# Kernel tuning notes

Measured on AMD Instinct MI355X. Metric: run time of the kernel, lower is better.

## Reference

```python
import jax, jax.numpy as jnp
import numpy as np

N, E, B = 50000, 600000, 512
IN, HID, META = 128, 128, 27


def _gcn_layer(h_in, W, b, src, dst, norm, n_nodes):
    # GCNConv: out = scatter_add_{dst}( norm * (x W)[src] ) + b
    h = h_in @ W  # [N, HID]
    msg = h[src] * norm[:, None]  # [E+N, HID] gather + scale
    out = jax.ops.segment_sum(msg, dst, num_segments=n_nodes)
    return out + b


def setup_inputs() -> dict:
    key = jax.random.key(0)
    ks = jax.random.split(key, 16)
    x = jax.random.normal(ks[0], (N, IN), dtype=jnp.float32)
    edge_index = jax.random.randint(ks[1], (2, E), 0, N, dtype=jnp.int64)
    batch = jnp.sort(jax.random.randint(ks[2], (N,), 0, B, dtype=jnp.int64))
    metadata = jax.random.normal(ks[3], (B, META), dtype=jnp.float32)
    def glorot(k, shape):
        lim = np.sqrt(6.0 / (shape[0] + shape[1]))
        return jax.random.uniform(k, shape, jnp.float32, -lim, lim)
    params = {
        'W1': glorot(ks[4], (IN, HID)),  'b1': jnp.zeros((HID,), jnp.float32),
        'W2': glorot(ks[5], (HID, HID)), 'b2': jnp.zeros((HID,), jnp.float32),
        'W3': glorot(ks[6], (HID, HID)), 'b3': jnp.zeros((HID,), jnp.float32),
        'Wh1': glorot(ks[7], (HID + META, HID)), 'bh1': jnp.zeros((HID,), jnp.float32),
        'Wh2': glorot(ks[8], (HID, 1)),  'bh2': jnp.zeros((1,), jnp.float32),
    }
    return {'x': x, 'edge_index': edge_index, 'batch': batch, 'metadata': metadata, **params}


def reference(x, edge_index, batch, metadata, W1, b1, W2, b2, W3, b3, Wh1, bh1, Wh2, bh2):
    n_nodes = x.shape[0]
    # add self loops (PyG GCNConv default)
    loops = jnp.arange(n_nodes, dtype=edge_index.dtype)
    src = jnp.concatenate([edge_index[0], loops])
    dst = jnp.concatenate([edge_index[1], loops])
    # symmetric degree normalization D^{-1/2} A_hat D^{-1/2}
    deg = jax.ops.segment_sum(jnp.ones_like(dst, dtype=x.dtype), dst, num_segments=n_nodes)
    dinv = jax.lax.rsqrt(jnp.maximum(deg, 1.0))  # self-loops guarantee deg >= 1
    norm = dinv[src] * dinv[dst]  # [E+N]
    h = jax.nn.relu(_gcn_layer(x, W1, b1, src, dst, norm, n_nodes))
    h = jax.nn.relu(_gcn_layer(h, W2, b2, src, dst, norm, n_nodes))
    h = jax.nn.relu(_gcn_layer(h, W3, b3, src, dst, norm, n_nodes))
    # global mean pool over graphs
    n_graphs = metadata.shape[0]
    summed = jax.ops.segment_sum(h, batch, num_segments=n_graphs)  # [B, HID]
    counts = jax.ops.segment_sum(jnp.ones((n_nodes,), x.dtype), batch, num_segments=n_graphs)
    emb = summed / jnp.maximum(counts, 1.0)[:, None]
    # MLP head
    z = jnp.concatenate([emb, metadata], axis=1)  # [B, HID+META]
    z = jax.nn.relu(z @ Wh1 + bh1)
    return z @ Wh2 + bh2  # [B, 1] raw logits
```

## Files before the change

kernel.cpp:

```cpp
#include <hip/hip_runtime.h>

#define NN 50000
#define NE 600000
#define NB 512
#define HD 128
#define NMETA 27
#define SCAN_BLOCKS ((NN + 255) / 256)

typedef __attribute__((ext_vector_type(8))) short short8;
typedef __attribute__((ext_vector_type(4))) float f32x4;

__device__ __forceinline__ float relu(float x) { return fmaxf(x, 0.0f); }

__device__ __forceinline__ unsigned short f2bf(float f) {
    unsigned u = __float_as_uint(f);
    unsigned r = u + 0x7FFFu + ((u >> 16) & 1u);
    return (unsigned short)(r >> 16);
}
__device__ __forceinline__ float bf2f(unsigned short v) {
    return __uint_as_float(((unsigned)v) << 16);
}

__global__ __launch_bounds__(256) void k_count(const int* __restrict__ dst, int* __restrict__ cnt) {
    int i = blockIdx.x * 256 + threadIdx.x;
    if (i < NE) atomicAdd(&cnt[dst[i]], 1);
}

__global__ __launch_bounds__(256) void k_scanA(const int* __restrict__ cnt, int* __restrict__ partial,
                                               int* __restrict__ blocksum, float* __restrict__ dinv) {
    const int t = threadIdx.x;
    const int i = blockIdx.x * 256 + t;
    int v = (i < NN) ? cnt[i] : 0;
    if (i < NN) dinv[i] = rsqrtf((float)v + 1.0f);
    __shared__ int s[256];
    s[t] = v;
    __syncthreads();
    for (int off = 1; off < 256; off <<= 1) {
        int u = (t >= off) ? s[t - off] : 0;
        __syncthreads();
        s[t] += u;
        __syncthreads();
    }
    if (i < NN) partial[i] = s[t] - v;
    if (t == 255) blocksum[blockIdx.x] = s[255];
}

__global__ __launch_bounds__(256) void k_scanB(const int* __restrict__ blocksum, int* __restrict__ blockoff) {
    const int t = threadIdx.x;
    int v = (t < SCAN_BLOCKS) ? blocksum[t] : 0;
    __shared__ int s[256];
    s[t] = v;
    __syncthreads();
    for (int off = 1; off < 256; off <<= 1) {
        int u = (t >= off) ? s[t - off] : 0;
        __syncthreads();
        s[t] += u;
        __syncthreads();
    }
    if (t < SCAN_BLOCKS) blockoff[t] = s[t] - v;
}

__global__ __launch_bounds__(256) void k_scanC(const int* __restrict__ partial, const int* __restrict__ blockoff,
                                               int* __restrict__ rowptr, int* __restrict__ cursor) {
    const int i = blockIdx.x * 256 + threadIdx.x;
    if (i < NN) {
        int rp = partial[i] + blockoff[i >> 8];
        rowptr[i] = rp;
        cursor[i] = rp;
    }
    if (i == 0) rowptr[NN] = NE;
}

__global__ __launch_bounds__(256) void k_fill(const int* __restrict__ src, const int* __restrict__ dst,
                                              int* __restrict__ cursor, int* __restrict__ csr_src) {
    int e = blockIdx.x * 256 + threadIdx.x;
    if (e >= NE) return;
    int s = src[e], d = dst[e];
    int pos = atomicAdd(&cursor[d], 1);
    csr_src[pos] = s;
}

__global__ __launch_bounds__(256) void k_castWt3(const float* __restrict__ W1, const float* __restrict__ W2,
                                                 const float* __restrict__ W3, unsigned short* __restrict__ Wt1,
                                                 unsigned short* __restrict__ Wt2, unsigned short* __restrict__ Wt3) {
    int i = blockIdx.x * 256 + threadIdx.x;
    if (i >= 3 * HD * HD) return;
    int which = i / (HD * HD);
    int r = i - which * (HD * HD);
    int k = r >> 7, n = r & 127;
    const float* W = (which == 0) ? W1 : (which == 1) ? W2 : W3;
    unsigned short* Wt = (which == 0) ? Wt1 : (which == 1) ? Wt2 : Wt3;
    Wt[n * HD + k] = f2bf(W[r]);
}

__global__ __launch_bounds__(256) void k_gemm_x(const float* __restrict__ X,
                                                const unsigned short* __restrict__ Wt,
                                                const float* __restrict__ dinv,
                                                unsigned short* __restrict__ T) {
    __shared__ unsigned short Ws[HD * HD];
    char* wsb = (char*)Ws;
    for (int i = threadIdx.x; i < HD * HD / 8; i += 256) {
        short8 v = ((const short8*)Wt)[i];
        int byte = i * 16;
        *(short8*)(wsb + (byte ^ (((byte >> 8) & 7) << 4))) = v;
    }
    __syncthreads();

    const int wave = threadIdx.x >> 6;
    const int lane = threadIdx.x & 63;
    const int lr = lane & 15;
    const int kh = lane >> 4;
    const int r0 = blockIdx.x * 64 + wave * 16;
    const float* arow = X + (size_t)min(r0 + lr, NN - 1) * HD + kh * 8;

    f32x4 acc[8] = {};
#pragma unroll
    for (int kk = 0; kk < 4; ++kk) {
        float4 a0 = *reinterpret_cast<const float4*>(arow + kk * 32);
        float4 a1 = *reinterpret_cast<const float4*>(arow + kk * 32 + 4);
        short8 af;
        af[0] = (short)f2bf(a0.x); af[1] = (short)f2bf(a0.y);
        af[2] = (short)f2bf(a0.z); af[3] = (short)f2bf(a0.w);
        af[4] = (short)f2bf(a1.x); af[5] = (short)f2bf(a1.y);
        af[6] = (short)f2bf(a1.z); af[7] = (short)f2bf(a1.w);
#pragma unroll
        for (int n = 0; n < 8; ++n) {
            int byte = (n * 16 + lr) * 256 + kk * 64 + kh * 16;
            short8 bf = *(const short8*)(wsb + (byte ^ (((byte >> 8) & 7) << 4)));
            acc[n] = __builtin_amdgcn_mfma_f32_16x16x32_bf16(af, bf, acc[n], 0, 0, 0);
        }
    }
    float dv[4];
#pragma unroll
    for (int r = 0; r < 4; ++r) {
        int row = r0 + kh * 4 + r;
        dv[r] = (row < NN) ? dinv[row] : 0.0f;
    }
#pragma unroll
    for (int n = 0; n < 8; ++n) {
#pragma unroll
        for (int r = 0; r < 4; ++r) {
            int row = r0 + kh * 4 + r;
            if (row < NN) T[(size_t)row * HD + n * 16 + lr] = f2bf(acc[n][r] * dv[r]);
        }
    }
}

template <int MODE>
__global__ __launch_bounds__(512, 8) void k_fused(const int* __restrict__ rowptr, const int* __restrict__ csr_src,
                                                  const unsigned short* __restrict__ Tin, const float* __restrict__ dinv,
                                                  const float* __restrict__ b, const unsigned short* __restrict__ Wt,
                                                  unsigned short* __restrict__ Out, const int* __restrict__ batch,
                                                  float* __restrict__ embsum) {
    __shared__ char smem[32 * 132 * 4 + 128];
    char* hsb = smem;
    float* hsf = (float*)smem;
    int* sg = (int*)(smem + 32 * 132 * 4);

    const int rl  = threadIdx.x >> 4;
    const int l16 = threadIdx.x & 15;
    const int row = blockIdx.x * 32 + rl;
    const int c   = l16 * 8;

    if (MODE == 2 && threadIdx.x < 32) {
        int rr = blockIdx.x * 32 + threadIdx.x;
        sg[threadIdx.x] = (rr < NN) ? batch[rr] : -1;
    }

    float acc[8] = {};

    if (row < NN) {
        const int lo = rowptr[row], hi = rowptr[row + 1];
        int j = lo;
        int sA0, sA1, sA2, sA3, sB0, sB1, sB2, sB3;
        bool haveA = (j + 3 < hi);
        if (haveA) { sA0 = csr_src[j]; sA1 = csr_src[j + 1]; sA2 = csr_src[j + 2]; sA3 = csr_src[j + 3]; }
        while (haveA) {
            const int jn = j + 4;
            const bool haveB = (jn + 3 < hi);
            if (haveB) { sB0 = csr_src[jn]; sB1 = csr_src[jn + 1]; sB2 = csr_src[jn + 2]; sB3 = csr_src[jn + 3]; }
            short8 t0 = *reinterpret_cast<const short8*>(Tin + (size_t)sA0 * HD + c);
            short8 t1 = *reinterpret_cast<const short8*>(Tin + (size_t)sA1 * HD + c);
            short8 t2 = *reinterpret_cast<const short8*>(Tin + (size_t)sA2 * HD + c);
            short8 t3 = *reinterpret_cast<const short8*>(Tin + (size_t)sA3 * HD + c);
#pragma unroll
            for (int i = 0; i < 8; ++i) {
                acc[i] += bf2f((unsigned short)t0[i]);
                acc[i] += bf2f((unsigned short)t1[i]);
                acc[i] += bf2f((unsigned short)t2[i]);
                acc[i] += bf2f((unsigned short)t3[i]);
            }
            j = jn;
            sA0 = sB0; sA1 = sB1; sA2 = sB2; sA3 = sB3;
            haveA = haveB;
        }
        for (; j < hi; ++j) {
            int s = csr_src[j];
            short8 tv = *reinterpret_cast<const short8*>(Tin + (size_t)s * HD + c);
#pragma unroll
            for (int i = 0; i < 8; ++i) acc[i] += bf2f((unsigned short)tv[i]);
        }
        const float di = dinv[row];
        short8 ts = *reinterpret_cast<const short8*>(Tin + (size_t)row * HD + c);
        float4 bb0 = *reinterpret_cast<const float4*>(b + c);
        float4 bb1 = *reinterpret_cast<const float4*>(b + c + 4);
        float h[8];
#pragma unroll
        for (int i = 0; i < 8; ++i) {
            float bbv = (i < 4) ? (&bb0.x)[i] : (&bb1.x)[i - 4];
            h[i] = relu(fmaf(di, acc[i] + bf2f((unsigned short)ts[i]), bbv));
        }
        if (MODE == 1) {
            short8 o;
#pragma unroll
            for (int i = 0; i < 8; ++i) o[i] = (short)f2bf(h[i]);
            int byte0 = rl * 256 + c * 2;
            *(short8*)(hsb + (byte0 ^ (((byte0 >> 8) & 7) << 4))) = o;
        } else {
            *(float4*)(&hsf[rl * 132 + c])     = make_float4(h[0], h[1], h[2], h[3]);
            *(float4*)(&hsf[rl * 132 + c + 4]) = make_float4(h[4], h[5], h[6], h[7]);
        }
    } else {
        if (MODE == 1) {
            short8 z = {0, 0, 0, 0, 0, 0, 0, 0};
            int byte0 = rl * 256 + c * 2;
            *(short8*)(hsb + (byte0 ^ (((byte0 >> 8) & 7) << 4))) = z;
        } else {
            float4 z = make_float4(0.f, 0.f, 0.f, 0.f);
            *(float4*)(&hsf[rl * 132 + c])     = z;
            *(float4*)(&hsf[rl * 132 + c + 4]) = z;
        }
    }
    __syncthreads();

    if (MODE == 1) {
        const int w = threadIdx.x >> 6;
        const int lane = threadIdx.x & 63;
        const int lr = lane & 15;
        const int kh = lane >> 4;
        f32x4 acc0 = {}, acc1 = {};
#pragma unroll
        for (int kk = 0; kk < 4; ++kk) {
            short8 bf = *reinterpret_cast<const short8*>(Wt + (size_t)(w * 16 + lr) * HD + kk * 32 + kh * 8);
            int byteA = lr * 256 + kk * 64 + kh * 16;
            int byteB = (16 + lr) * 256 + kk * 64 + kh * 16;
            short8 af0 = *(const short8*)(hsb + (byteA ^ (((byteA >> 8) & 7) << 4)));
            short8 af1 = *(const short8*)(hsb + (byteB ^ (((byteB >> 8) & 7) << 4)));
            acc0 = __builtin_amdgcn_mfma_f32_16x16x32_bf16(af0, bf, acc0, 0, 0, 0);
            acc1 = __builtin_amdgcn_mfma_f32_16x16x32_bf16(af1, bf, acc1, 0, 0, 0);
        }
#pragma unroll
        for (int r = 0; r < 4; ++r) {
            int row0 = blockIdx.x * 32 + kh * 4 + r;
            int row1 = row0 + 16;
            if (row0 < NN) Out[(size_t)row0 * HD + w * 16 + lr] = f2bf(acc0[r] * dinv[row0]);
            if (row1 < NN) Out[(size_t)row1 * HD + w * 16 + lr] = f2bf(acc1[r] * dinv[row1]);
        }
    } else {
        if (threadIdx.x < HD) {
            const int cc = threadIdx.x;
            float a = 0.f;
            int gcur = -1;
#pragma unroll 8
            for (int r = 0; r < 32; ++r) {
                int g = sg[r];
                if (g != gcur) {
                    if (gcur >= 0) atomicAdd(&embsum[gcur * HD + cc], a);
                    a = 0.f;
                    gcur = g;
                }
                a += hsf[r * 132 + cc];
            }
            if (gcur >= 0) atomicAdd(&embsum[gcur * HD + cc], a);
        }
    }
}

__global__ __launch_bounds__(128) void k_head(const float* __restrict__ embsum, const int* __restrict__ batch,
                                              const float* __restrict__ meta,
                                              const float* __restrict__ Wh1, const float* __restrict__ bh1,
                                              const float* __restrict__ Wh2, const float* __restrict__ bh2,
                                              float* __restrict__ out) {
    int g = blockIdx.x;
    int c = threadIdx.x;
    int l = 0, r = NN;
    while (l < r) { int m = (l + r) >> 1; if (batch[m] < g) l = m + 1; else r = m; }
    int lo = l;
    r = NN;
    while (l < r) { int m = (l + r) >> 1; if (batch[m] < g + 1) l = m + 1; else r = m; }
    int hi = l;
    float rcp = 1.0f / (float)max(hi - lo, 1);

    __shared__ float emb[HD];
    __shared__ float mt[NMETA];
    emb[c] = embsum[g * HD + c] * rcp;
    if (c < NMETA) mt[c] = meta[g * NMETA + c];
    __syncthreads();

    float z = bh1[c];
    float z0 = 0.f, z1 = 0.f, z2 = 0.f, z3 = 0.f;
    for (int k = 0; k < HD; k += 4) {
        z0 = fmaf(emb[k],     Wh1[k * HD + c],       z0);
        z1 = fmaf(emb[k + 1], Wh1[(k + 1) * HD + c], z1);
        z2 = fmaf(emb[k + 2], Wh1[(k + 2) * HD + c], z2);
        z3 = fmaf(emb[k + 3], Wh1[(k + 3) * HD + c], z3);
    }
    for (int k = 0; k < NMETA; ++k) z = fmaf(mt[k], Wh1[(HD + k) * HD + c], z);
    z += (z0 + z1) + (z2 + z3);
    z = relu(z);
    __shared__ float red[HD];
    red[c] = z * Wh2[c];
    __syncthreads();
    for (int st = 64; st > 0; st >>= 1) {
        if (c < st) red[c] += red[c + st];
        __syncthreads();
    }
    if (c == 0) out[g] = red[0] + bh2[0];
}

extern "C" void kernel_launch(void* const* d_in, const int* in_sizes, int n_in,
                              void* d_out, int out_size, void* d_ws, size_t ws_size,
                              hipStream_t stream) {
    const float* x     = (const float*)d_in[0];
    const int*   ei    = (const int*)d_in[1];
    const int*   src   = ei;
    const int*   dst   = ei + NE;
    const int*   batch = (const int*)d_in[2];
    const float* meta  = (const float*)d_in[3];
    const float* W1 = (const float*)d_in[4];  const float* b1 = (const float*)d_in[5];
    const float* W2 = (const float*)d_in[6];  const float* b2 = (const float*)d_in[7];
    const float* W3 = (const float*)d_in[8];  const float* b3 = (const float*)d_in[9];
    const float* Wh1 = (const float*)d_in[10]; const float* bh1 = (const float*)d_in[11];
    const float* Wh2 = (const float*)d_in[12]; const float* bh2 = (const float*)d_in[13];
    float* out = (float*)d_out;

    int*   csr_src  = (int*)d_ws;
    int*   cnt      = csr_src + NE;
    int*   partial  = cnt + NN;
    int*   blocksum = partial + NN;
    int*   blockoff = blocksum + 256;
    int*   rowptr   = blockoff + 256;
    int*   cursor   = rowptr + NN + 8;
    float* dinv     = (float*)(cursor + NN);
    float* embsum   = dinv + NN;
    unsigned short* Ta  = (unsigned short*)(embsum + NB * HD);
    unsigned short* Tc  = Ta + (size_t)NN * HD;
    unsigned short* Wt1 = Tc + (size_t)NN * HD;
    unsigned short* Wt2 = Wt1 + HD * HD;
    unsigned short* Wt3 = Wt2 + HD * HD;

    const int GEMM_GRID  = (NN + 63) / 64;
    const int FUSED_GRID = (NN + 31) / 32;
    const int CWT_GRID   = (3 * HD * HD + 255) / 256;

    hipMemsetAsync(cnt, 0, NN * sizeof(int), stream);
    hipMemsetAsync(embsum, 0, NB * HD * sizeof(float), stream);
    k_count<<<(NE + 255) / 256, 256, 0, stream>>>(dst, cnt);
    k_scanA<<<SCAN_BLOCKS, 256, 0, stream>>>(cnt, partial, blocksum, dinv);
    k_scanB<<<1, 256, 0, stream>>>(blocksum, blockoff);
    k_scanC<<<SCAN_BLOCKS, 256, 0, stream>>>(partial, blockoff, rowptr, cursor);
    k_fill<<<(NE + 255) / 256, 256, 0, stream>>>(src, dst, cursor, csr_src);

    k_castWt3<<<CWT_GRID, 256, 0, stream>>>(W1, W2, W3, Wt1, Wt2, Wt3);

    k_gemm_x<<<GEMM_GRID, 256, 0, stream>>>(x, Wt1, dinv, Ta);
    k_fused<1><<<FUSED_GRID, 512, 0, stream>>>(rowptr, csr_src, Ta, dinv, b1, Wt2, Tc, nullptr, nullptr);
    k_fused<1><<<FUSED_GRID, 512, 0, stream>>>(rowptr, csr_src, Tc, dinv, b2, Wt3, Ta, nullptr, nullptr);
    k_fused<2><<<FUSED_GRID, 512, 0, stream>>>(rowptr, csr_src, Ta, dinv, b3, nullptr, nullptr, batch, embsum);

    k_head<<<NB, 128, 0, stream>>>(embsum, batch, meta, Wh1, bh1, Wh2, bh2, out);
}
```

Measured before the change: 294.1 us.

## Split fused gather+GEMM into column-paneled gather and separate MFMA GEMM kernels

Replaces the fused aggregate-then-transform kernel with two kernels per layer. The gather kernel splits the 128 feature columns into 8 panels of 16 across blocks and spreads each row's edges over 8 lanes, then reduces with shuffles. A separate bf16 MFMA GEMM with W staged in swizzled shared memory applies the next layer's weights. The aim is better cache locality for the gathered source rows and more parallelism per row. The cost is extra launches, a round trip of the intermediate H through global memory, and 8x re-reading of rowptr and csr_src.

```diff
diff --git a/kernel.cpp b/kernel.cpp
--- a/kernel.cpp
+++ b/kernel.cpp
@@ -146,132 +146,132 @@
     }
 }
 
+__global__ __launch_bounds__(256) void k_gemm_h(const unsigned short* __restrict__ A,
+                                                const unsigned short* __restrict__ Wt,
+                                                const float* __restrict__ dinv,
+                                                unsigned short* __restrict__ T) {
+    __shared__ unsigned short Ws[HD * HD];
+    char* wsb = (char*)Ws;
+    for (int i = threadIdx.x; i < HD * HD / 8; i += 256) {
+        short8 v = ((const short8*)Wt)[i];
+        int byte = i * 16;
+        *(short8*)(wsb + (byte ^ (((byte >> 8) & 7) << 4))) = v;
+    }
+    __syncthreads();
+
+    const int wave = threadIdx.x >> 6;
+    const int lane = threadIdx.x & 63;
+    const int lr = lane & 15;
+    const int kh = lane >> 4;
+    const int r0 = blockIdx.x * 64 + wave * 16;
+    const unsigned short* arow = A + (size_t)min(r0 + lr, NN - 1) * HD + kh * 8;
+
+    f32x4 acc[8] = {};
+#pragma unroll
+    for (int kk = 0; kk < 4; ++kk) {
+        short8 af = *reinterpret_cast<const short8*>(arow + kk * 32);
+#pragma unroll
+        for (int n = 0; n < 8; ++n) {
+            int byte = (n * 16 + lr) * 256 + kk * 64 + kh * 16;
+            short8 bf = *(const short8*)(wsb + (byte ^ (((byte >> 8) & 7) << 4)));
+            acc[n] = __builtin_amdgcn_mfma_f32_16x16x32_bf16(af, bf, acc[n], 0, 0, 0);
+        }
+    }
+    float dv[4];
+#pragma unroll
+    for (int r = 0; r < 4; ++r) {
+        int row = r0 + kh * 4 + r;
+        dv[r] = (row < NN) ? dinv[row] : 0.0f;
+    }
+#pragma unroll
+    for (int n = 0; n < 8; ++n) {
+#pragma unroll
+        for (int r = 0; r < 4; ++r) {
+            int row = r0 + kh * 4 + r;
+            if (row < NN) T[(size_t)row * HD + n * 16 + lr] = f2bf(acc[n][r] * dv[r]);
+        }
+    }
+}
+
 template <int MODE>
-__global__ __launch_bounds__(512, 8) void k_fused(const int* __restrict__ rowptr, const int* __restrict__ csr_src,
-                                                  const unsigned short* __restrict__ Tin, const float* __restrict__ dinv,
-                                                  const float* __restrict__ b, const unsigned short* __restrict__ Wt,
-                                                  unsigned short* __restrict__ Out, const int* __restrict__ batch,
-                                                  float* __restrict__ embsum) {
-    __shared__ char smem[32 * 132 * 4 + 128];
-    char* hsb = smem;
-    float* hsf = (float*)smem;
-    int* sg = (int*)(smem + 32 * 132 * 4);
-
+__global__ __launch_bounds__(512, 8) void k_gath(const int* __restrict__ rowptr, const int* __restrict__ csr_src,
+                                                 const unsigned short* __restrict__ Tin, const float* __restrict__ dinv,
+                                                 const float* __restrict__ b, unsigned short* __restrict__ H,
+                                                 const int* __restrict__ batch, float* __restrict__ embsum) {
+    const int panel = blockIdx.x & 7;
+    const int rb    = blockIdx.x >> 3;
     const int rl  = threadIdx.x >> 4;
-    const int l16 = threadIdx.x & 15;
-    const int row = blockIdx.x * 32 + rl;
-    const int c   = l16 * 8;
-
+    const int li  = threadIdx.x & 15;
+    const int es  = li >> 1;
+    const int ch  = li & 1;
+    const int row = rb * 32 + rl;
+    const int c   = panel * 16 + ch * 8;
+
+    __shared__ float hs[32][17];
+    __shared__ int sg[32];
     if (MODE == 2 && threadIdx.x < 32) {
-        int rr = blockIdx.x * 32 + threadIdx.x;
+        int rr = rb * 32 + threadIdx.x;
         sg[threadIdx.x] = (rr < NN) ? batch[rr] : -1;
     }
 
     float acc[8] = {};
-
     if (row < NN) {
         const int lo = rowptr[row], hi = rowptr[row + 1];
-        int j = lo;
-        int sA0, sA1, sA2, sA3, sB0, sB1, sB2, sB3;
-        bool haveA = (j + 3 < hi);
-        if (haveA) { sA0 = csr_src[j]; sA1 = csr_src[j + 1]; sA2 = csr_src[j + 2]; sA3 = csr_src[j + 3]; }
-        while (haveA) {
-            const int jn = j + 4;
-            const bool haveB = (jn + 3 < hi);
-            if (haveB) { sB0 = csr_src[jn]; sB1 = csr_src[jn + 1]; sB2 = csr_src[jn + 2]; sB3 = csr_src[jn + 3]; }
-            short8 t0 = *reinterpret_cast<const short8*>(Tin + (size_t)sA0 * HD + c);
-            short8 t1 = *reinterpret_cast<const short8*>(Tin + (size_t)sA1 * HD + c);
-            short8 t2 = *reinterpret_cast<const short8*>(Tin + (size_t)sA2 * HD + c);
-            short8 t3 = *reinterpret_cast<const short8*>(Tin + (size_t)sA3 * HD + c);
-#pragma unroll
-            for (int i = 0; i < 8; ++i) {
-                acc[i] += bf2f((unsigned short)t0[i]);
-                acc[i] += bf2f((unsigned short)t1[i]);
-                acc[i] += bf2f((unsigned short)t2[i]);
-                acc[i] += bf2f((unsigned short)t3[i]);
-            }
-            j = jn;
-            sA0 = sB0; sA1 = sB1; sA2 = sB2; sA3 = sB3;
-            haveA = haveB;
-        }
-        for (; j < hi; ++j) {
+        for (int j = lo + es; j < hi; j += 8) {
             int s = csr_src[j];
             short8 tv = *reinterpret_cast<const short8*>(Tin + (size_t)s * HD + c);
 #pragma unroll
             for (int i = 0; i < 8; ++i) acc[i] += bf2f((unsigned short)tv[i]);
         }
-        const float di = dinv[row];
-        short8 ts = *reinterpret_cast<const short8*>(Tin + (size_t)row * HD + c);
-        float4 bb0 = *reinterpret_cast<const float4*>(b + c);
-        float4 bb1 = *reinterpret_cast<const float4*>(b + c + 4);
-        float h[8];
-#pragma unroll
-        for (int i = 0; i < 8; ++i) {
-            float bbv = (i < 4) ? (&bb0.x)[i] : (&bb1.x)[i - 4];
-            h[i] = relu(fmaf(di, acc[i] + bf2f((unsigned short)ts[i]), bbv));
-        }
-        if (MODE == 1) {
-            short8 o;
-#pragma unroll
-            for (int i = 0; i < 8; ++i) o[i] = (short)f2bf(h[i]);
-            int byte0 = rl * 256 + c * 2;
-            *(short8*)(hsb + (byte0 ^ (((byte0 >> 8) & 7) << 4))) = o;
-        } else {
-            *(float4*)(&hsf[rl * 132 + c])     = make_float4(h[0], h[1], h[2], h[3]);
-            *(float4*)(&hsf[rl * 132 + c + 4]) = make_float4(h[4], h[5], h[6], h[7]);
-        }
-    } else {
-        if (MODE == 1) {
-            short8 z = {0, 0, 0, 0, 0, 0, 0, 0};
-            int byte0 = rl * 256 + c * 2;
-            *(short8*)(hsb + (byte0 ^ (((byte0 >> 8) & 7) << 4))) = z;
-        } else {
-            float4 z = make_float4(0.f, 0.f, 0.f, 0.f);
-            *(float4*)(&hsf[rl * 132 + c])     = z;
-            *(float4*)(&hsf[rl * 132 + c + 4]) = z;
-        }
-    }
-    __syncthreads();
-
-    if (MODE == 1) {
-        const int w = threadIdx.x >> 6;
-        const int lane = threadIdx.x & 63;
-        const int lr = lane & 15;
-        const int kh = lane >> 4;
-        f32x4 acc0 = {}, acc1 = {};
-#pragma unroll
-        for (int kk = 0; kk < 4; ++kk) {
-            short8 bf = *reinterpret_cast<const short8*>(Wt + (size_t)(w * 16 + lr) * HD + kk * 32 + kh * 8);
-            int byteA = lr * 256 + kk * 64 + kh * 16;
-            int byteB = (16 + lr) * 256 + kk * 64 + kh * 16;
-            short8 af0 = *(const short8*)(hsb + (byteA ^ (((byteA >> 8) & 7) << 4)));
-            short8 af1 = *(const short8*)(hsb + (byteB ^ (((byteB >> 8) & 7) << 4)));
-            acc0 = __builtin_amdgcn_mfma_f32_16x16x32_bf16(af0, bf, acc0, 0, 0, 0);
-            acc1 = __builtin_amdgcn_mfma_f32_16x16x32_bf16(af1, bf, acc1, 0, 0, 0);
-        }
-#pragma unroll
-        for (int r = 0; r < 4; ++r) {
-            int row0 = blockIdx.x * 32 + kh * 4 + r;
-            int row1 = row0 + 16;
-            if (row0 < NN) Out[(size_t)row0 * HD + w * 16 + lr] = f2bf(acc0[r] * dinv[row0]);
-            if (row1 < NN) Out[(size_t)row1 * HD + w * 16 + lr] = f2bf(acc1[r] * dinv[row1]);
-        }
-    } else {
-        if (threadIdx.x < HD) {
+    }
+#pragma unroll
+    for (int i = 0; i < 8; ++i) {
+        acc[i] += __shfl_xor(acc[i], 2);
+        acc[i] += __shfl_xor(acc[i], 4);
+        acc[i] += __shfl_xor(acc[i], 8);
+    }
+    if (es == 0) {
+        if (row < NN) {
+            float di = dinv[row];
+            short8 ts = *reinterpret_cast<const short8*>(Tin + (size_t)row * HD + c);
+            float4 bb0 = *reinterpret_cast<const float4*>(b + c);
+            float4 bb1 = *reinterpret_cast<const float4*>(b + c + 4);
+            float h[8];
+#pragma unroll
+            for (int i = 0; i < 8; ++i) {
+                float bbv = (i < 4) ? (&bb0.x)[i] : (&bb1.x)[i - 4];
+                h[i] = relu(fmaf(di, acc[i] + bf2f((unsigned short)ts[i]), bbv));
+            }
+            if (MODE == 1) {
+                short8 o;
+#pragma unroll
+                for (int i = 0; i < 8; ++i) o[i] = (short)f2bf(h[i]);
+                *reinterpret_cast<short8*>(H + (size_t)row * HD + c) = o;
+            } else {
+#pragma unroll
+                for (int i = 0; i < 8; ++i) hs[rl][ch * 8 + i] = h[i];
+            }
+        } else if (MODE == 2) {
+#pragma unroll
+            for (int i = 0; i < 8; ++i) hs[rl][ch * 8 + i] = 0.f;
+        }
+    }
+    if (MODE == 2) {
+        __syncthreads();
+        if (threadIdx.x < 16) {
             const int cc = threadIdx.x;
             float a = 0.f;
             int gcur = -1;
-#pragma unroll 8
             for (int r = 0; r < 32; ++r) {
                 int g = sg[r];
                 if (g != gcur) {
-                    if (gcur >= 0) atomicAdd(&embsum[gcur * HD + cc], a);
+                    if (gcur >= 0) atomicAdd(&embsum[gcur * HD + panel * 16 + cc], a);
                     a = 0.f;
                     gcur = g;
                 }
-                a += hsf[r * 132 + cc];
+                a += hs[r][cc];
             }
-            if (gcur >= 0) atomicAdd(&embsum[gcur * HD + cc], a);
+            if (gcur >= 0) atomicAdd(&embsum[gcur * HD + panel * 16 + cc], a);
         }
     }
 }
@@ -345,13 +345,15 @@
     float* embsum   = dinv + NN;
     unsigned short* Ta  = (unsigned short*)(embsum + NB * HD);
     unsigned short* Tc  = Ta + (size_t)NN * HD;
-    unsigned short* Wt1 = Tc + (size_t)NN * HD;
+    unsigned short* Hb  = Tc + (size_t)NN * HD;
+    unsigned short* Wt1 = Hb + (size_t)NN * HD;
     unsigned short* Wt2 = Wt1 + HD * HD;
     unsigned short* Wt3 = Wt2 + HD * HD;
 
-    const int GEMM_GRID  = (NN + 63) / 64;
-    const int FUSED_GRID = (NN + 31) / 32;
-    const int CWT_GRID   = (3 * HD * HD + 255) / 256;
+    const int GEMM_GRID = (NN + 63) / 64;
+    const int ROWBLKS   = (NN + 31) / 32;
+    const int GATH_GRID = ROWBLKS * 8;
+    const int CWT_GRID  = (3 * HD * HD + 255) / 256;
 
     hipMemsetAsync(cnt, 0, NN * sizeof(int), stream);
     hipMemsetAsync(embsum, 0, NB * HD * sizeof(float), stream);
@@ -364,9 +366,11 @@
     k_castWt3<<<CWT_GRID, 256, 0, stream>>>(W1, W2, W3, Wt1, Wt2, Wt3);
 
     k_gemm_x<<<GEMM_GRID, 256, 0, stream>>>(x, Wt1, dinv, Ta);
-    k_fused<1><<<FUSED_GRID, 512, 0, stream>>>(rowptr, csr_src, Ta, dinv, b1, Wt2, Tc, nullptr, nullptr);
-    k_fused<1><<<FUSED_GRID, 512, 0, stream>>>(rowptr, csr_src, Tc, dinv, b2, Wt3, Ta, nullptr, nullptr);
-    k_fused<2><<<FUSED_GRID, 512, 0, stream>>>(rowptr, csr_src, Ta, dinv, b3, nullptr, nullptr, batch, embsum);
+    k_gath<1><<<GATH_GRID, 512, 0, stream>>>(rowptr, csr_src, Ta, dinv, b1, Hb, nullptr, nullptr);
+    k_gemm_h<<<GEMM_GRID, 256, 0, stream>>>(Hb, Wt2, dinv, Tc);
+    k_gath<1><<<GATH_GRID, 512, 0, stream>>>(rowptr, csr_src, Tc, dinv, b2, Hb, nullptr, nullptr);
+    k_gemm_h<<<GEMM_GRID, 256, 0, stream>>>(Hb, Wt3, dinv, Ta);
+    k_gath<2><<<GATH_GRID, 512, 0, stream>>>(rowptr, csr_src, Ta, dinv, b3, nullptr, batch, embsum);
 
     k_head<<<NB, 128, 0, stream>>>(embsum, batch, meta, Wh1, bh1, Wh2, bh2, out);
 }
```

Result: slower. 400.6 us (+36.2%).
